# Optimization experiments

Measured on AMD Instinct MI355X. Metric: run time of the kernel, lower is better.

Reference implementation:

```python
import jax, jax.numpy as jnp
import numpy as np
import math

DIM = 1536; NH = 12; HD = 128
F, H, W = 6, 30, 30
S = F * H * W
B = 1
K_LEN = 9900  # hardcoded k_lens in the source forward
EPS_NORM = 1e-6


def _rope_tables(max_len=1024, d=HD):
    # Wan rope_params: three tables of widths d-4*(d//6), 2*(d//6), 2*(d//6)
    # -> cos/sin tables of half-widths 22, 21, 21 (concat = d//2 = 64)
    def ang(dd):
        inv = 1.0 / (10000.0 ** (np.arange(0, dd, 2, dtype=np.float64) / dd))
        return np.outer(np.arange(max_len, dtype=np.float64), inv)
    a = np.concatenate([ang(d - 4 * (d // 6)), ang(2 * (d // 6)), ang(2 * (d // 6))], axis=1)
    return np.cos(a).astype(np.float32), np.sin(a).astype(np.float32)


def setup_inputs() -> dict:
    key = jax.random.key(0)
    ks = jax.random.split(key, 5)
    s = 1.0 / math.sqrt(DIM)
    cos, sin = _rope_tables()
    return {
        "x": jax.random.normal(ks[0], (B, S, DIM), jnp.float32),
        "q_w": jax.random.normal(ks[1], (DIM, DIM), jnp.float32) * s,
        "q_b": jnp.zeros((DIM,), jnp.float32),
        "k_w": jax.random.normal(ks[2], (DIM, DIM), jnp.float32) * s,
        "k_b": jnp.zeros((DIM,), jnp.float32),
        "v_w": jax.random.normal(ks[3], (DIM, DIM), jnp.float32) * s,
        "v_b": jnp.zeros((DIM,), jnp.float32),
        "o_w": jax.random.normal(ks[4], (DIM, DIM), jnp.float32) * s,
        "o_b": jnp.zeros((DIM,), jnp.float32),
        "norm_q_w": jnp.ones((DIM,), jnp.float32),
        "norm_k_w": jnp.ones((DIM,), jnp.float32),
        "freqs_cos": jnp.asarray(cos),
        "freqs_sin": jnp.asarray(sin),
        "grid_f": F, "grid_h": H, "grid_w": W,
    }


def rms_norm(x, w):
    # RMSNorm over full model dim, computed in fp32 (as in source)
    xf = x.astype(jnp.float32)
    xn = xf * jax.lax.rsqrt(jnp.mean(xf * xf, axis=-1, keepdims=True) + EPS_NORM)
    return xn.astype(x.dtype) * w


def rope_apply(x, cos, sin, f, h, w):
    # x: [B,S,N,D]; rotate consecutive pairs with 3D-factorized (f,h,w) freqs
    Bb, Ss, Nn, Dd = x.shape
    c = Dd // 2
    sp = [c - 2 * (c // 3), c // 3, c // 3]  # 22, 21, 21

    def grid(tab):
        tf = tab[:, :sp[0]]
        th = tab[:, sp[0]:sp[0] + sp[1]]
        tw = tab[:, sp[0] + sp[1]:]
        g = jnp.concatenate([
            jnp.broadcast_to(tf[:f, None, None, :], (f, h, w, sp[0])),
            jnp.broadcast_to(th[None, :h, None, :], (f, h, w, sp[1])),
            jnp.broadcast_to(tw[None, None, :w, :], (f, h, w, sp[2])),
        ], axis=-1)
        return g.reshape(f * h * w, 1, c)  # [S,1,c] (broadcast over heads)

    gc, gs = grid(cos), grid(sin)
    xp = x.astype(jnp.float32).reshape(Bb, Ss, Nn, c, 2)
    xr, xi = xp[..., 0], xp[..., 1]
    orr = xr * gc - xi * gs
    oii = xr * gs + xi * gc
    return jnp.stack([orr, oii], axis=-1).reshape(Bb, Ss, Nn, Dd).astype(x.dtype)


def attention(q, k, v, k_len):
    # full attention (window_size=(-1,-1)) with keys masked beyond k_len
    scale = 1.0 / math.sqrt(q.shape[-1])
    att = jnp.einsum('bqnd,bknd->bnqk', q, k) * scale
    valid = jnp.arange(k.shape[1]) < k_len
    att = jnp.where(valid[None, None, None, :], att, jnp.finfo(att.dtype).min)
    p = jax.nn.softmax(att, axis=-1)
    return jnp.einsum('bnqk,bknd->bqnd', p, v)


def reference(x, q_w, q_b, k_w, k_b, v_w, v_b, o_w, o_b, norm_q_w, norm_k_w, freqs_cos, freqs_sin, grid_f, grid_h, grid_w):
    Bb, Ss, _ = x.shape
    q = rms_norm(x @ q_w.T + q_b, norm_q_w).reshape(Bb, Ss, NH, HD)
    k = rms_norm(x @ k_w.T + k_b, norm_k_w).reshape(Bb, Ss, NH, HD)
    v = (x @ v_w.T + v_b).reshape(Bb, Ss, NH, HD)
    q = rope_apply(q, freqs_cos, freqs_sin, grid_f, grid_h, grid_w)
    k = rope_apply(k, freqs_cos, freqs_sin, grid_f, grid_h, grid_w)
    o = attention(q, k, v, K_LEN).reshape(Bb, Ss, NH * HD)
    return o @ o_w.T + o_b
```

## Files before the change

### kernel.cpp

```cpp
#include <hip/hip_runtime.h>

#define DIM 1536
#define NH 12
#define HD 128
#define S_LEN 5400
#define SPAD 5440
#define MPAD 5504
#define NQKV 4608
#define EPS_NORM 1e-6f

typedef __bf16 bf16_t;
typedef __bf16 bf16x8 __attribute__((ext_vector_type(8)));
typedef __bf16 bf16x4 __attribute__((ext_vector_type(4)));
typedef float  f32x4  __attribute__((ext_vector_type(4)));
typedef float  f32x16 __attribute__((ext_vector_type(16)));

#define GLOAD_LDS16(gp, lp) __builtin_amdgcn_global_load_lds( \
    (__attribute__((address_space(1))) void*)(void*)(gp),     \
    (__attribute__((address_space(3))) void*)(lp), 16, 0, 0)


__global__ __launch_bounds__(256) void cvt_x_kernel(const float* __restrict__ x,
                                                    bf16_t* __restrict__ xb) {
  size_t base = ((size_t)blockIdx.x * 256 + threadIdx.x) * 4;
  if (base >= (size_t)MPAD * DIM) return;
  size_t row = base / DIM;
  float4 v = make_float4(0.f, 0.f, 0.f, 0.f);
  if (row < S_LEN) v = *(const float4*)&x[base];
  bf16x4 o; o[0] = (__bf16)v.x; o[1] = (__bf16)v.y; o[2] = (__bf16)v.z; o[3] = (__bf16)v.w;
  *(bf16x4*)&xb[base] = o;
}

__global__ __launch_bounds__(256) void cvt_wqkv_kernel(const float* __restrict__ qw,
                                                       const float* __restrict__ kw,
                                                       const float* __restrict__ vw,
                                                       bf16_t* __restrict__ wb) {
  size_t base = ((size_t)blockIdx.x * 256 + threadIdx.x) * 4;
  if (base >= (size_t)NQKV * DIM) return;
  int row = (int)(base / DIM);
  int col = (int)(base - (size_t)row * DIM);
  const float* src; int rr = row;
  if (rr >= 3072)      { src = vw; rr -= 3072; }
  else if (rr >= 1536) { src = kw; rr -= 1536; }
  else                 { src = qw; }
  float4 v = *(const float4*)&src[(size_t)rr * DIM + col];
  bf16x4 o; o[0] = (__bf16)v.x; o[1] = (__bf16)v.y; o[2] = (__bf16)v.z; o[3] = (__bf16)v.w;
  *(bf16x4*)&wb[base] = o;
}

__global__ __launch_bounds__(256) void cvt_wo_kernel(const float* __restrict__ w,
                                                     bf16_t* __restrict__ wb) {
  size_t base = ((size_t)blockIdx.x * 256 + threadIdx.x) * 4;
  if (base >= (size_t)DIM * DIM) return;
  float4 v = *(const float4*)&w[base];
  bf16x4 o; o[0] = (__bf16)v.x; o[1] = (__bf16)v.y; o[2] = (__bf16)v.z; o[3] = (__bf16)v.w;
  *(bf16x4*)&wb[base] = o;
}


template<bool OUT_BF16>
__global__ __launch_bounds__(256) void gemm_bt_kernel(
    const bf16_t* __restrict__ A, const bf16_t* __restrict__ B, void* __restrict__ C,
    const float* __restrict__ bias0, const float* __restrict__ bias1,
    const float* __restrict__ bias2, int M, int N, int K, int Mvalid) {
  __shared__ bf16_t As[128 * 32];
  __shared__ bf16_t Bs[128 * 32];
  int tid = threadIdx.x;
  int lane = tid & 63, wave = tid >> 6, quad = lane >> 4, l16 = lane & 15;
  int m0 = blockIdx.y * 128, n0 = blockIdx.x * 128;
  int wm = (wave >> 1) * 64, wn = (wave & 1) * 64;
  const bf16_t* Ab = A + (size_t)m0 * K;
  const bf16_t* Bb = B + (size_t)n0 * K;
  f32x4 acc[4][4] = {};
  for (int kt = 0; kt < K; kt += 32) {
    __syncthreads();
#pragma unroll
    for (int i = 0; i < 2; i++) {
      int eo = (i * 256 + tid) * 8;
      int row = eo >> 5, col = eo & 31;
      GLOAD_LDS16(Ab + (size_t)row * K + kt + col, &As[eo]);
      GLOAD_LDS16(Bb + (size_t)row * K + kt + col, &Bs[eo]);
    }
    __syncthreads();
    bf16x8 af[4], bfr[4];
#pragma unroll
    for (int i = 0; i < 4; i++)
      af[i] = *(const bf16x8*)&As[(wm + i * 16 + l16) * 32 + quad * 8];
#pragma unroll
    for (int j = 0; j < 4; j++)
      bfr[j] = *(const bf16x8*)&Bs[(wn + j * 16 + l16) * 32 + quad * 8];
#pragma unroll
    for (int i = 0; i < 4; i++)
#pragma unroll
      for (int j = 0; j < 4; j++)
        acc[i][j] = __builtin_amdgcn_mfma_f32_16x16x32_bf16(af[i], bfr[j], acc[i][j], 0, 0, 0);
  }
#pragma unroll
  for (int j = 0; j < 4; j++) {
    int n = n0 + wn + j * 16 + l16;
    float bias = (n < 1536) ? bias0[n] : (n < 3072) ? bias1[n - 1536] : bias2[n - 3072];
#pragma unroll
    for (int i = 0; i < 4; i++) {
#pragma unroll
      for (int r = 0; r < 4; r++) {
        int m = m0 + wm + i * 16 + quad * 4 + r;
        float v = acc[i][j][r] + bias;
        if (OUT_BF16) {
          ((bf16_t*)C)[(size_t)m * N + n] = (__bf16)v;
        } else {
          if (m < Mvalid) ((float*)C)[(size_t)m * N + n] = v;
        }
      }
    }
  }
}


__global__ __launch_bounds__(256) void rope_qk_kernel(
    const bf16_t* __restrict__ qkv, const float* __restrict__ nqw,
    const float* __restrict__ nkw, const float* __restrict__ fcos,
    const float* __restrict__ fsin, bf16_t* __restrict__ qout,
    bf16_t* __restrict__ kout) {
  int s = blockIdx.x;
  int tid = threadIdx.x;
  bool valid = s < S_LEN;
  int f = s / 900, hh = (s / 30) % 30, ww = s % 30;
  __shared__ float red[4];
  for (int which = 0; which < 2; which++) {
    const bf16_t* src = qkv + (size_t)s * NQKV + which * DIM;
    const float* nw = which ? nkw : nqw;
    bf16_t* dst = (which ? kout : qout) + (size_t)s * DIM;
    float osc = which ? 1.0f : 0.08838834764831845f;
    float v[6]; float ss = 0.f;
#pragma unroll
    for (int i = 0; i < 6; i++) {
      v[i] = valid ? (float)src[tid * 6 + i] : 0.f;
      ss += v[i] * v[i];
    }
#pragma unroll
    for (int off = 32; off >= 1; off >>= 1) ss += __shfl_down(ss, off);
    if ((tid & 63) == 0) red[tid >> 6] = ss;
    __syncthreads();
    float tot = red[0] + red[1] + red[2] + red[3];
    float rn = rsqrtf(tot * (1.f / DIM) + EPS_NORM);
    __syncthreads();
#pragma unroll
    for (int i = 0; i < 3; i++) {
      int e0 = tid * 6 + 2 * i;
      int p = e0 >> 1;
      int cc = p & 63;
      int pos = (cc < 22) ? f : (cc < 43) ? hh : ww;
      float c = fcos[pos * 64 + cc], sn = fsin[pos * 64 + cc];
      float xr = v[2 * i] * rn * nw[e0];
      float xi = v[2 * i + 1] * rn * nw[e0 + 1];
      dst[e0]     = (__bf16)((xr * c - xi * sn) * osc);
      dst[e0 + 1] = (__bf16)((xr * sn + xi * c) * osc);
    }
  }
}


__global__ __launch_bounds__(256) void v_transpose_kernel(const bf16_t* __restrict__ qkv,
                                                          bf16_t* __restrict__ vt) {
  __shared__ bf16_t tile[64][136];
  int h = blockIdx.y, s0 = blockIdx.x * 64, tid = threadIdx.x;
#pragma unroll
  for (int it = 0; it < 4; it++) {
    int eo = (it * 256 + tid) * 8;
    int row = eo >> 7, col = eo & 127;
    int s = s0 + row;
    bf16x8 val = {};
    if (s < S_LEN) val = *(const bf16x8*)&qkv[(size_t)s * NQKV + 3072 + h * HD + col];
    *(bf16x8*)&tile[row][col] = val;
  }
  __syncthreads();
  int d = tid & 127, j0 = (tid >> 7) * 32;
  bf16x8 outv[4];
#pragma unroll
  for (int b = 0; b < 4; b++)
#pragma unroll
    for (int j = 0; j < 8; j++) outv[b][j] = tile[j0 + b * 8 + j][d];
  size_t base = ((size_t)h * HD + d) * SPAD + s0 + j0;
#pragma unroll
  for (int b = 0; b < 4; b++) *(bf16x8*)&vt[base + b * 8] = outv[b];
}


__global__ __launch_bounds__(256, 2) void flash_attn_kernel(
    const bf16_t* __restrict__ q, const bf16_t* __restrict__ k,
    const bf16_t* __restrict__ vt, bf16_t* __restrict__ o) {
  __shared__ bf16_t Ks[64 * 128];
  __shared__ bf16_t Vs[64 * 128];
  __shared__ bf16_t Pw[4][32 * 64];
  int head = blockIdx.y;
  int s0 = blockIdx.x * 128;
  int tid = threadIdx.x, w = tid >> 6, lane = tid & 63;
  int l31 = lane & 31, hh = lane >> 5;

  bf16x8 bq[8];
  {
    const bf16_t* qp = &q[(size_t)(s0 + w * 32 + l31) * DIM + head * HD + hh * 8];
#pragma unroll
    for (int kc = 0; kc < 8; kc++) bq[kc] = *(const bf16x8*)(qp + kc * 16);
  }

  float m_i = -1e30f, l_i = 0.f;
  f32x16 oacc[4] = {};

  for (int kt = 0; kt < SPAD; kt += 64) {
    __syncthreads();
#pragma unroll
    for (int it = 0; it < 4; it++) {
      int slot = it * 256 + tid;
      int row = slot >> 4, pc = slot & 15;
      int c = pc ^ (row & 15);
      GLOAD_LDS16(k + (size_t)(kt + row) * DIM + head * HD + c * 8, &Ks[slot * 8]);
    }
#pragma unroll
    for (int it = 0; it < 4; it++) {
      int slot = it * 256 + tid;
      int row = slot >> 4, pc = slot & 15;
      int cp = pc ^ (row & 15);
      int d = 2 * row + (cp >> 3);
      GLOAD_LDS16(vt + ((size_t)head * HD + d) * SPAD + kt + (cp & 7) * 8, &Vs[slot * 8]);
    }
    __syncthreads();

    f32x16 sacc[2] = {};
#pragma unroll
    for (int ns = 0; ns < 2; ns++) {
      int row = ns * 32 + l31;
#pragma unroll
      for (int kc = 0; kc < 8; kc++) {
        int pc = (kc * 2 + hh) ^ (row & 15);
        bf16x8 ak = *(const bf16x8*)&Ks[row * 128 + pc * 8];
        sacc[ns] = __builtin_amdgcn_mfma_f32_32x32x16_bf16(ak, bq[kc], sacc[ns], 0, 0, 0);
      }
    }

    if (kt + 64 > S_LEN) {
#pragma unroll
      for (int ns = 0; ns < 2; ns++)
#pragma unroll
        for (int r = 0; r < 16; r++) {
          int kvg = kt + ns * 32 + (r & 3) + 8 * (r >> 2) + 4 * hh;
          if (kvg >= S_LEN) sacc[ns][r] = -1e30f;
        }
    }

    float mx = -1e30f;
#pragma unroll
    for (int ns = 0; ns < 2; ns++)
#pragma unroll
      for (int r = 0; r < 16; r++) mx = fmaxf(mx, sacc[ns][r]);
    mx = fmaxf(mx, __shfl_xor(mx, 32));
    float mn = fmaxf(m_i, mx);
    float al = __expf(m_i - mn);
    m_i = mn;
    float rs = 0.f;
#pragma unroll
    for (int ns = 0; ns < 2; ns++)
#pragma unroll
      for (int r = 0; r < 16; r++) {
        float p = __expf(sacc[ns][r] - mn);
        rs += p;
        sacc[ns][r] = p;
      }
    rs += __shfl_xor(rs, 32);
    l_i = l_i * al + rs;
#pragma unroll
    for (int dt = 0; dt < 4; dt++)
#pragma unroll
      for (int r = 0; r < 16; r++) oacc[dt][r] *= al;

#pragma unroll
    for (int ns = 0; ns < 2; ns++)
#pragma unroll
      for (int t = 0; t < 4; t++) {
        bf16x4 pk;
#pragma unroll
        for (int r4 = 0; r4 < 4; r4++) pk[r4] = (__bf16)sacc[ns][t * 4 + r4];
        int c8 = ns * 8 + 2 * t + hh;
        int pc8 = c8 ^ (l31 & 15);
        *(bf16x4*)&Pw[w][l31 * 64 + pc8 * 4] = pk;
      }

#pragma unroll
    for (int kvc = 0; kvc < 4; kvc++) {
      int c8a = kvc * 4 + hh * 2;
      bf16x4 plo = *(const bf16x4*)&Pw[w][l31 * 64 + ((c8a) ^ (l31 & 15)) * 4];
      bf16x4 phi = *(const bf16x4*)&Pw[w][l31 * 64 + ((c8a + 1) ^ (l31 & 15)) * 4];
      bf16x8 bp;
#pragma unroll
      for (int j = 0; j < 4; j++) { bp[j] = plo[j]; bp[j + 4] = phi[j]; }
#pragma unroll
      for (int dt = 0; dt < 4; dt++) {
        int d = dt * 32 + l31;
        int r = d >> 1;
        int cp = ((d & 1) << 3) | (kvc * 2 + hh);
        int pc = cp ^ (r & 15);
        bf16x8 av = *(const bf16x8*)&Vs[r * 128 + pc * 8];
        oacc[dt] = __builtin_amdgcn_mfma_f32_32x32x16_bf16(av, bp, oacc[dt], 0, 0, 0);
      }
    }
  }

  float inv = 1.f / l_i;
  int qr = lane >> 1, seg = lane & 1;
  int srow = s0 + w * 32 + qr;
#pragma unroll
  for (int half = 0; half < 2; half++) {
#pragma unroll
    for (int dl = 0; dl < 2; dl++) {
      int dt = half * 2 + dl;
#pragma unroll
      for (int t = 0; t < 4; t++) {
        bf16x4 v;
#pragma unroll
        for (int r4 = 0; r4 < 4; r4++) v[r4] = (__bf16)(oacc[dt][t * 4 + r4] * inv);
        int c8 = dl * 8 + 2 * t + hh;
        int pc8 = c8 ^ (l31 & 15);
        *(bf16x4*)&Pw[w][l31 * 64 + pc8 * 4] = v;
      }
    }
#pragma unroll
    for (int i = 0; i < 4; i++) {
      int c8 = seg * 8 + 2 * i;
      bf16x4 lo = *(const bf16x4*)&Pw[w][qr * 64 + ((c8) ^ (qr & 15)) * 4];
      bf16x4 hi = *(const bf16x4*)&Pw[w][qr * 64 + ((c8 + 1) ^ (qr & 15)) * 4];
      bf16x8 val;
#pragma unroll
      for (int j = 0; j < 4; j++) { val[j] = lo[j]; val[j + 4] = hi[j]; }
      if (srow < S_LEN)
        *(bf16x8*)&o[(size_t)srow * DIM + head * HD + half * 64 + seg * 32 + i * 8] = val;
    }
    __syncthreads();
  }
}


extern "C" void kernel_launch(void* const* d_in, const int* in_sizes, int n_in,
                              void* d_out, int out_size, void* d_ws, size_t ws_size,
                              hipStream_t stream) {
  const float* x    = (const float*)d_in[0];
  const float* q_w  = (const float*)d_in[1];
  const float* q_b  = (const float*)d_in[2];
  const float* k_w  = (const float*)d_in[3];
  const float* k_b  = (const float*)d_in[4];
  const float* v_w  = (const float*)d_in[5];
  const float* v_b  = (const float*)d_in[6];
  const float* o_w  = (const float*)d_in[7];
  const float* o_b  = (const float*)d_in[8];
  const float* nqw  = (const float*)d_in[9];
  const float* nkw  = (const float*)d_in[10];
  const float* fcos = (const float*)d_in[11];
  const float* fsin = (const float*)d_in[12];

  char* ws = (char*)d_ws;
  bf16_t* xb   = (bf16_t*)(ws + 0);
  bf16_t* wqkv = (bf16_t*)(ws + 16908288);
  bf16_t* wob  = (bf16_t*)(ws + 31064064);
  bf16_t* qkv  = (bf16_t*)(ws + 35782656);
  bf16_t* qb   = (bf16_t*)(ws + 86507520);
  bf16_t* kb   = (bf16_t*)(ws + 103415808);
  bf16_t* vtb  = (bf16_t*)(ws + 0);
  bf16_t* aob  = (bf16_t*)(ws + 35782656);

  cvt_x_kernel<<<(MPAD * DIM / 4 + 255) / 256, 256, 0, stream>>>(x, xb);
  cvt_wqkv_kernel<<<(NQKV * DIM / 4 + 255) / 256, 256, 0, stream>>>(q_w, k_w, v_w, wqkv);
  cvt_wo_kernel<<<(DIM * DIM / 4 + 255) / 256, 256, 0, stream>>>(o_w, wob);

  gemm_bt_kernel<true><<<dim3(NQKV / 128, MPAD / 128), 256, 0, stream>>>(
      xb, wqkv, qkv, q_b, k_b, v_b, MPAD, NQKV, DIM, MPAD);

  rope_qk_kernel<<<MPAD, 256, 0, stream>>>(qkv, nqw, nkw, fcos, fsin, qb, kb);
  v_transpose_kernel<<<dim3(SPAD / 64, NH), 256, 0, stream>>>(qkv, vtb);

  flash_attn_kernel<<<dim3(MPAD / 128, NH), 256, 0, stream>>>(qb, kb, vtb, aob);

  gemm_bt_kernel<false><<<dim3(DIM / 128, MPAD / 128), 256, 0, stream>>>(
      aob, wob, d_out, o_b, o_b, o_b, MPAD, DIM, DIM, S_LEN);
}
```

Measured before the change: 691.6 us.

## Double-buffer LDS tiles in GEMM and flash attention, add lazy softmax rescale

Both the projection GEMM and the flash-attention kernel now keep two LDS buffers and issue the global-to-LDS loads for the next K tile while computing on the current one, leaving one barrier per iteration. The goal is to hide global memory latency behind MFMA work. The attention kernel also skips the running-max rescale of the output accumulator unless the new max exceeds the old by more than 8, and raises wave priority around the MFMA sections. Doubling the buffers roughly doubles LDS use for K/V, which can reduce occupancy, and the lazy rescale lets unnormalized exponentials grow as large as e^8 before correction.

```diff
diff --git a/kernel.cpp b/kernel.cpp
--- a/kernel.cpp
+++ b/kernel.cpp
@@ -63,8 +63,8 @@
     const bf16_t* __restrict__ A, const bf16_t* __restrict__ B, void* __restrict__ C,
     const float* __restrict__ bias0, const float* __restrict__ bias1,
     const float* __restrict__ bias2, int M, int N, int K, int Mvalid) {
-  __shared__ bf16_t As[128 * 32];
-  __shared__ bf16_t Bs[128 * 32];
+  __shared__ bf16_t As[2][128 * 32];
+  __shared__ bf16_t Bs[2][128 * 32];
   int tid = threadIdx.x;
   int lane = tid & 63, wave = tid >> 6, quad = lane >> 4, l16 = lane & 15;
   int m0 = blockIdx.y * 128, n0 = blockIdx.x * 128;
@@ -72,28 +72,45 @@
   const bf16_t* Ab = A + (size_t)m0 * K;
   const bf16_t* Bb = B + (size_t)n0 * K;
   f32x4 acc[4][4] = {};
-  for (int kt = 0; kt < K; kt += 32) {
-    __syncthreads();
-#pragma unroll
-    for (int i = 0; i < 2; i++) {
-      int eo = (i * 256 + tid) * 8;
-      int row = eo >> 5, col = eo & 31;
-      GLOAD_LDS16(Ab + (size_t)row * K + kt + col, &As[eo]);
-      GLOAD_LDS16(Bb + (size_t)row * K + kt + col, &Bs[eo]);
-    }
-    __syncthreads();
+
+  int eo0 = tid * 8;
+  int row0 = eo0 >> 5, col0 = eo0 & 31;
+  int eo1 = (256 + tid) * 8;
+  int row1 = eo1 >> 5, col1 = eo1 & 31;
+
+  GLOAD_LDS16(Ab + (size_t)row0 * K + col0, &As[0][eo0]);
+  GLOAD_LDS16(Bb + (size_t)row0 * K + col0, &Bs[0][eo0]);
+  GLOAD_LDS16(Ab + (size_t)row1 * K + col1, &As[0][eo1]);
+  GLOAD_LDS16(Bb + (size_t)row1 * K + col1, &Bs[0][eo1]);
+  asm volatile("s_waitcnt vmcnt(0)" ::: "memory");
+  __builtin_amdgcn_s_barrier();
+  __builtin_amdgcn_sched_barrier(0);
+
+  int KT = K >> 5;
+  for (int t = 0; t < KT; t++) {
+    int cur = t & 1;
+    if (t + 1 < KT) {
+      int kn = (t + 1) << 5;
+      GLOAD_LDS16(Ab + (size_t)row0 * K + kn + col0, &As[cur ^ 1][eo0]);
+      GLOAD_LDS16(Bb + (size_t)row0 * K + kn + col0, &Bs[cur ^ 1][eo0]);
+      GLOAD_LDS16(Ab + (size_t)row1 * K + kn + col1, &As[cur ^ 1][eo1]);
+      GLOAD_LDS16(Bb + (size_t)row1 * K + kn + col1, &Bs[cur ^ 1][eo1]);
+    }
     bf16x8 af[4], bfr[4];
 #pragma unroll
     for (int i = 0; i < 4; i++)
-      af[i] = *(const bf16x8*)&As[(wm + i * 16 + l16) * 32 + quad * 8];
+      af[i] = *(const bf16x8*)&As[cur][(wm + i * 16 + l16) * 32 + quad * 8];
 #pragma unroll
     for (int j = 0; j < 4; j++)
-      bfr[j] = *(const bf16x8*)&Bs[(wn + j * 16 + l16) * 32 + quad * 8];
+      bfr[j] = *(const bf16x8*)&Bs[cur][(wn + j * 16 + l16) * 32 + quad * 8];
 #pragma unroll
     for (int i = 0; i < 4; i++)
 #pragma unroll
       for (int j = 0; j < 4; j++)
         acc[i][j] = __builtin_amdgcn_mfma_f32_16x16x32_bf16(af[i], bfr[j], acc[i][j], 0, 0, 0);
+    asm volatile("s_waitcnt vmcnt(0) lgkmcnt(0)" ::: "memory");
+    __builtin_amdgcn_s_barrier();
+    __builtin_amdgcn_sched_barrier(0);
   }
 #pragma unroll
   for (int j = 0; j < 4; j++) {
@@ -189,8 +206,8 @@
 __global__ __launch_bounds__(256, 2) void flash_attn_kernel(
     const bf16_t* __restrict__ q, const bf16_t* __restrict__ k,
     const bf16_t* __restrict__ vt, bf16_t* __restrict__ o) {
-  __shared__ bf16_t Ks[64 * 128];
-  __shared__ bf16_t Vs[64 * 128];
+  __shared__ bf16_t Ks[2][64 * 128];
+  __shared__ bf16_t Vs[2][64 * 128];
   __shared__ bf16_t Pw[4][32 * 64];
   int head = blockIdx.y;
   int s0 = blockIdx.x * 128;
@@ -207,36 +224,63 @@
   float m_i = -1e30f, l_i = 0.f;
   f32x16 oacc[4] = {};
 
-  for (int kt = 0; kt < SPAD; kt += 64) {
-    __syncthreads();
-#pragma unroll
-    for (int it = 0; it < 4; it++) {
-      int slot = it * 256 + tid;
-      int row = slot >> 4, pc = slot & 15;
-      int c = pc ^ (row & 15);
-      GLOAD_LDS16(k + (size_t)(kt + row) * DIM + head * HD + c * 8, &Ks[slot * 8]);
-    }
-#pragma unroll
-    for (int it = 0; it < 4; it++) {
-      int slot = it * 256 + tid;
-      int row = slot >> 4, pc = slot & 15;
-      int cp = pc ^ (row & 15);
-      int d = 2 * row + (cp >> 3);
-      GLOAD_LDS16(vt + ((size_t)head * HD + d) * SPAD + kt + (cp & 7) * 8, &Vs[slot * 8]);
-    }
-    __syncthreads();
+  const int NT = SPAD / 64;
+
+#pragma unroll
+  for (int it = 0; it < 4; it++) {
+    int slot = it * 256 + tid;
+    int row = slot >> 4, pc = slot & 15;
+    int c = pc ^ (row & 15);
+    GLOAD_LDS16(k + (size_t)row * DIM + head * HD + c * 8, &Ks[0][slot * 8]);
+  }
+#pragma unroll
+  for (int it = 0; it < 4; it++) {
+    int slot = it * 256 + tid;
+    int row = slot >> 4, pc = slot & 15;
+    int cp = pc ^ (row & 15);
+    int d = 2 * row + (cp >> 3);
+    GLOAD_LDS16(vt + ((size_t)head * HD + d) * SPAD + (cp & 7) * 8, &Vs[0][slot * 8]);
+  }
+  asm volatile("s_waitcnt vmcnt(0)" ::: "memory");
+  __builtin_amdgcn_s_barrier();
+  __builtin_amdgcn_sched_barrier(0);
+
+  for (int t = 0; t < NT; t++) {
+    int kt = t * 64;
+    int cur = t & 1;
+
+    if (t + 1 < NT) {
+      int kn = kt + 64;
+#pragma unroll
+      for (int it = 0; it < 4; it++) {
+        int slot = it * 256 + tid;
+        int row = slot >> 4, pc = slot & 15;
+        int c = pc ^ (row & 15);
+        GLOAD_LDS16(k + (size_t)(kn + row) * DIM + head * HD + c * 8, &Ks[cur ^ 1][slot * 8]);
+      }
+#pragma unroll
+      for (int it = 0; it < 4; it++) {
+        int slot = it * 256 + tid;
+        int row = slot >> 4, pc = slot & 15;
+        int cp = pc ^ (row & 15);
+        int d = 2 * row + (cp >> 3);
+        GLOAD_LDS16(vt + ((size_t)head * HD + d) * SPAD + kn + (cp & 7) * 8, &Vs[cur ^ 1][slot * 8]);
+      }
+    }
 
     f32x16 sacc[2] = {};
+    __builtin_amdgcn_s_setprio(1);
 #pragma unroll
     for (int ns = 0; ns < 2; ns++) {
       int row = ns * 32 + l31;
 #pragma unroll
       for (int kc = 0; kc < 8; kc++) {
         int pc = (kc * 2 + hh) ^ (row & 15);
-        bf16x8 ak = *(const bf16x8*)&Ks[row * 128 + pc * 8];
+        bf16x8 ak = *(const bf16x8*)&Ks[cur][row * 128 + pc * 8];
         sacc[ns] = __builtin_amdgcn_mfma_f32_32x32x16_bf16(ak, bq[kc], sacc[ns], 0, 0, 0);
       }
     }
+    __builtin_amdgcn_s_setprio(0);
 
     if (kt + 64 > S_LEN) {
 #pragma unroll
@@ -254,37 +298,41 @@
 #pragma unroll
       for (int r = 0; r < 16; r++) mx = fmaxf(mx, sacc[ns][r]);
     mx = fmaxf(mx, __shfl_xor(mx, 32));
-    float mn = fmaxf(m_i, mx);
-    float al = __expf(m_i - mn);
-    m_i = mn;
+    if (!__all(mx - m_i <= 8.f)) {
+      float mn = fmaxf(m_i, mx);
+      float al = __expf(m_i - mn);
+      l_i *= al;
+#pragma unroll
+      for (int dt = 0; dt < 4; dt++)
+#pragma unroll
+        for (int r = 0; r < 16; r++) oacc[dt][r] *= al;
+      m_i = mn;
+    }
     float rs = 0.f;
 #pragma unroll
     for (int ns = 0; ns < 2; ns++)
 #pragma unroll
       for (int r = 0; r < 16; r++) {
-        float p = __expf(sacc[ns][r] - mn);
+        float p = __expf(sacc[ns][r] - m_i);
         rs += p;
         sacc[ns][r] = p;
       }
     rs += __shfl_xor(rs, 32);
-    l_i = l_i * al + rs;
-#pragma unroll
-    for (int dt = 0; dt < 4; dt++)
-#pragma unroll
-      for (int r = 0; r < 16; r++) oacc[dt][r] *= al;
+    l_i += rs;
 
 #pragma unroll
     for (int ns = 0; ns < 2; ns++)
 #pragma unroll
-      for (int t = 0; t < 4; t++) {
+      for (int tt = 0; tt < 4; tt++) {
         bf16x4 pk;
 #pragma unroll
-        for (int r4 = 0; r4 < 4; r4++) pk[r4] = (__bf16)sacc[ns][t * 4 + r4];
-        int c8 = ns * 8 + 2 * t + hh;
+        for (int r4 = 0; r4 < 4; r4++) pk[r4] = (__bf16)sacc[ns][tt * 4 + r4];
+        int c8 = ns * 8 + 2 * tt + hh;
         int pc8 = c8 ^ (l31 & 15);
         *(bf16x4*)&Pw[w][l31 * 64 + pc8 * 4] = pk;
       }
 
+    __builtin_amdgcn_s_setprio(1);
 #pragma unroll
     for (int kvc = 0; kvc < 4; kvc++) {
       int c8a = kvc * 4 + hh * 2;
@@ -299,10 +347,15 @@
         int r = d >> 1;
         int cp = ((d & 1) << 3) | (kvc * 2 + hh);
         int pc = cp ^ (r & 15);
-        bf16x8 av = *(const bf16x8*)&Vs[r * 128 + pc * 8];
+        bf16x8 av = *(const bf16x8*)&Vs[cur][r * 128 + pc * 8];
         oacc[dt] = __builtin_amdgcn_mfma_f32_32x32x16_bf16(av, bp, oacc[dt], 0, 0, 0);
       }
     }
+    __builtin_amdgcn_s_setprio(0);
+
+    asm volatile("s_waitcnt vmcnt(0) lgkmcnt(0)" ::: "memory");
+    __builtin_amdgcn_s_barrier();
+    __builtin_amdgcn_sched_barrier(0);
   }
 
   float inv = 1.f / l_i;
@@ -314,11 +367,11 @@
     for (int dl = 0; dl < 2; dl++) {
       int dt = half * 2 + dl;
 #pragma unroll
-      for (int t = 0; t < 4; t++) {
+      for (int tt = 0; tt < 4; tt++) {
         bf16x4 v;
 #pragma unroll
-        for (int r4 = 0; r4 < 4; r4++) v[r4] = (__bf16)(oacc[dt][t * 4 + r4] * inv);
-        int c8 = dl * 8 + 2 * t + hh;
+        for (int r4 = 0; r4 < 4; r4++) v[r4] = (__bf16)(oacc[dt][tt * 4 + r4] * inv);
+        int c8 = dl * 8 + 2 * tt + hh;
         int pc8 = c8 ^ (l31 & 15);
         *(bf16x4*)&Pw[w][l31 * 64 + pc8 * 4] = v;
       }
```

Result: no change. 689.8 us (-0.3%).
